# Kernel tuning notes

Measured on AMD Instinct MI355X. Metric: run time of the kernel, lower is better.

The kernel has to match this reference:

```python
import jax, jax.numpy as jnp
import numpy as np

EPS = 1e-5

def _ln(x, g, b):
    mu = x.mean(-1, keepdims=True)
    var = ((x - mu) ** 2).mean(-1, keepdims=True)
    return (x - mu) * jax.lax.rsqrt(var + EPS) * g + b

def setup_inputs() -> dict:
    B, K, D, H, T = 64, 64, 128, 128, 4
    key = jax.random.key(0)
    ks = jax.random.split(key, 20)
    s = 0.02
    inp = {
        "slots": jax.random.normal(ks[0], (B, K, D), jnp.float32),
        "edge_probs": jax.random.uniform(ks[1], (B, K, K), jnp.float32),
        "edge_types": jax.random.uniform(ks[2], (B, K, K, T), jnp.float32),
        # f_self: LayerNorm(D) -> Linear(D,H) -> ReLU -> Linear(H,D)
        "ls_g": jnp.ones((D,), jnp.float32),
        "ls_b": jnp.zeros((D,), jnp.float32),
        "ws1": jax.random.normal(ks[3], (D, H), jnp.float32) * s,
        "bs1": jnp.zeros((H,), jnp.float32),
        "ws2": jax.random.normal(ks[4], (H, D), jnp.float32) * s,
        "bs2": jnp.zeros((D,), jnp.float32),
        # f_inter[tau]: Linear(2D,H) -> ReLU -> Linear(H,H) -> ReLU -> Linear(H,D), stacked over T
        "wi1": jax.random.normal(ks[5], (T, 2 * D, H), jnp.float32) * s,
        "bi1": jnp.zeros((T, H), jnp.float32),
        "wi2": jax.random.normal(ks[6], (T, H, H), jnp.float32) * s,
        "bi2": jnp.zeros((T, H), jnp.float32),
        "wi3": jax.random.normal(ks[7], (T, H, D), jnp.float32) * s,
        "bi3": jnp.zeros((T, D), jnp.float32),
        # update_mlp: LayerNorm(2D) -> Linear(2D,H) -> ReLU -> Linear(H,D)
        "lu_g": jnp.ones((2 * D,), jnp.float32),
        "lu_b": jnp.zeros((2 * D,), jnp.float32),
        "wu1": jax.random.normal(ks[8], (2 * D, H), jnp.float32) * s,
        "bu1": jnp.zeros((H,), jnp.float32),
        "wu2": jax.random.normal(ks[9], (H, D), jnp.float32) * s,
        "bu2": jnp.zeros((D,), jnp.float32),
    }
    return inp

NUM_MP = 2

def reference(slots, edge_probs, edge_types, ls_g, ls_b, ws1, bs1, ws2, bs2,
              wi1, bi1, wi2, bi2, wi3, bi3, lu_g, lu_b, wu1, bu1, wu2, bu2):
    B, K, D = slots.shape
    T = edge_types.shape[-1]
    h = slots
    for _ in range(NUM_MP):
        # f_self
        delta_self = jax.nn.relu(_ln(h, ls_g, ls_b) @ ws1 + bs1) @ ws2 + bs2
        # all-pairs features: cat[b,i,j] = [h[b,i] (sender), h[b,j] (receiver)]
        sender = jnp.broadcast_to(h[:, :, None, :], (B, K, K, D))
        receiver = jnp.broadcast_to(h[:, None, :, :], (B, K, K, D))
        pair = jnp.concatenate([sender, receiver], axis=-1)  # [B,K,K,2D]
        delta_inter = jnp.zeros_like(h)
        for tau in range(T):
            x = jax.nn.relu(pair @ wi1[tau] + bi1[tau])
            x = jax.nn.relu(x @ wi2[tau] + bi2[tau])
            eff = x @ wi3[tau] + bi3[tau]  # [B,K,K,D]
            w = edge_probs[..., None] * edge_types[..., tau, None]  # [B,K,K,1]
            delta_inter = delta_inter + (eff * w).sum(axis=1)  # sum over sender i
        combined = jnp.concatenate([h + delta_self, delta_inter], axis=-1)
        update = jax.nn.relu(_ln(combined, lu_g, lu_b) @ wu1 + bu1) @ wu2 + bu2
        h = h + update  # residual=True
    return h
```

## Files before the change

### kernel.cpp

```cpp
#include <hip/hip_runtime.h>
#include <hip/hip_fp16.h>

#define BATCH 64
#define KSLOT 64
#define DDIM  128
#define HDIM  128
#define TTYPE 4
#define NSLOT (BATCH*KSLOT)
#define EPSLN 1e-5f
#define YROW  544

typedef _Float16 v8h __attribute__((ext_vector_type(8)));
typedef _Float16 v4h __attribute__((ext_vector_type(4)));
typedef float    v4f __attribute__((ext_vector_type(4)));

__device__ __forceinline__ float waveAllSum(float v) {
    #pragma unroll
    for (int m = 1; m < 64; m <<= 1) v += __shfl_xor(v, m, 64);
    return v;
}

__global__ __launch_bounds__(256) void k_wconv(
        const float* __restrict__ ws1, const float* __restrict__ wi1,
        const float* __restrict__ ws2, const float* __restrict__ wu1,
        const float* __restrict__ wu2, const float* __restrict__ wi3,
        const float* __restrict__ wi2, const float* __restrict__ bi1,
        const float* __restrict__ bi3,
        const float* __restrict__ ep, const float* __restrict__ et,
        __half* __restrict__ ws1T, __half* __restrict__ wi1catT,
        __half* __restrict__ ws2T, __half* __restrict__ wu1T,
        __half* __restrict__ wu2T, __half* __restrict__ w3catT,
        __half* __restrict__ w2T16, float* __restrict__ biascat,
        __half* __restrict__ wPre) {
    __shared__ __align__(16) float tile[128*132];
    int bx = blockIdx.x, tid = threadIdx.x;
    if (bx >= 22) {
        int bx2 = bx - 22, tau = bx2 & 3, b = bx2 >> 2;
        const float* epb = ep + (size_t)b*4096;
        const float* etb = et + (size_t)b*4096*TTYPE + tau;
        __half* dst = wPre + ((size_t)tau*BATCH + b)*4096;
        for (int idx = tid; idx < 4096; idx += 256)
            dst[idx] = __float2half(epb[idx] * etb[(size_t)idx*TTYPE]);
        return;
    }
    if (bx == 21) {
        for (int idx = tid; idx < 128*32; idx += 256) {
            int o = idx >> 5, c = idx & 31;
            w3catT[(size_t)o*YROW + 512 + c] = (c < 4) ? __float2half(bi3[c*DDIM + o]) : __float2half(0.f);
        }
        for (int idx = tid; idx < 1024; idx += 256) {
            int th = idx >> 7, o = idx & 127;
            biascat[idx] = (th & 1) ? bi1[(th>>1)*HDIM + o] : 0.f;
        }
        return;
    }
    const float* src; __half* dst; int dstride = 128, dcol = 0;
    if (bx == 0)      { src = ws1; dst = ws1T; }
    else if (bx <= 8) { int th = bx-1, tau = th>>1, half = th&1;
                        src = wi1 + ((size_t)tau*256 + half*128)*128;
                        dst = wi1catT + (size_t)th*128*128; }
    else if (bx == 9) { src = ws2; dst = ws2T; }
    else if (bx ==10) { src = wu2; dst = wu2T; }
    else if (bx <=12) { int hh = bx-11; src = wu1 + (size_t)hh*128*128;
                        dst = wu1T; dstride = 256; dcol = hh*128; }
    else if (bx <=16) { int tau = bx-13; src = wi3 + (size_t)tau*16384;
                        dst = w3catT; dstride = YROW; dcol = tau*128; }
    else              { int tau = bx-17; src = wi2 + (size_t)tau*16384;
                        dst = w2T16 + (size_t)tau*16384; }
    for (int idx = tid; idx < 4096; idx += 256) {
        int r = idx >> 5, c4 = idx & 31;
        *(float4*)&tile[r*132 + c4*4] = *(const float4*)&src[(size_t)r*128 + c4*4];
    }
    __syncthreads();
    for (int idx = tid; idx < 8192; idx += 256) {
        int n = idx >> 6, kp = idx & 63;
        __half2 p = __floats2half2_rn(tile[(2*kp)*132 + n], tile[(2*kp+1)*132 + n]);
        *(__half2*)&dst[(size_t)n*dstride + dcol + 2*kp] = p;
    }
}

__global__ __launch_bounds__(256) void k_front(
        const float* __restrict__ h,
        const __half* __restrict__ wi1catT, const float* __restrict__ biascat,
        const float* __restrict__ ls_g, const float* __restrict__ ls_b,
        const __half* __restrict__ ws1T, const float* __restrict__ bs1,
        const __half* __restrict__ ws2T, const float* __restrict__ bs2,
        __half* __restrict__ AtCt, float* __restrict__ comb128) {
    __shared__ __align__(16) char smem[17152];
    int tid = threadIdx.x, lane = tid & 63, w = tid >> 6;
    int n = lane & 15, quad = lane >> 4;
    int row0 = blockIdx.x*16, nb = blockIdx.y;
    if (nb < 4) {
        _Float16* Ha = (_Float16*)smem;
        for (int u = tid; u < 16*32; u += 256) {
            int r = u >> 5, c4 = (u & 31)*4;
            float4 f = *(const float4*)&h[(size_t)(row0 + r)*128 + c4];
            *(__half2*)&Ha[r*136 + c4]     = __floats2half2_rn(f.x, f.y);
            *(__half2*)&Ha[r*136 + c4 + 2] = __floats2half2_rn(f.z, f.w);
        }
        __syncthreads();
        v8h bfrag[4][4];
        #pragma unroll
        for (int ot = 0; ot < 4; ot++) {
            int col = nb*256 + w*64 + ot*16 + n;
            #pragma unroll
            for (int ks = 0; ks < 4; ks++)
                bfrag[ot][ks] = *(const v8h*)&wi1catT[(size_t)col*128 + ks*32 + quad*8];
        }
        v4f acc[4];
        #pragma unroll
        for (int ot = 0; ot < 4; ot++) {
            float b0 = biascat[nb*256 + w*64 + ot*16 + n];
            acc[ot] = (v4f){b0, b0, b0, b0};
        }
        #pragma unroll
        for (int ks = 0; ks < 4; ks++) {
            v8h a = *(const v8h*)&Ha[n*136 + ks*32 + quad*8];
            #pragma unroll
            for (int ot = 0; ot < 4; ot++)
                acc[ot] = __builtin_amdgcn_mfma_f32_16x16x32_f16(a, bfrag[ot][ks], acc[ot], 0, 0, 0);
        }
        __syncthreads();
        _Float16* Ot = (_Float16*)smem;
        #pragma unroll
        for (int ot = 0; ot < 4; ot++)
            #pragma unroll
            for (int r = 0; r < 4; r++)
                Ot[(quad*4 + r)*264 + w*64 + ot*16 + n] = (_Float16)acc[ot][r];
        __syncthreads();
        #pragma unroll
        for (int u = 0; u < 2; u++) {
            int k = tid + u*256;
            int r = k >> 5, c8 = (k & 31)*8;
            *(v8h*)&AtCt[(size_t)(row0 + r)*1024 + nb*256 + c8] = *(const v8h*)&Ot[r*264 + c8];
        }
    } else {
        float*    Hrow = (float*)smem;
        _Float16* Xa = (_Float16*)(smem + 8448);
        _Float16* Tt = (_Float16*)(smem + 8448 + 4352);
        v8h b1[2][4], b2[2][4];
        #pragma unroll
        for (int ot = 0; ot < 2; ot++) {
            int col = w*32 + ot*16 + n;
            #pragma unroll
            for (int ks = 0; ks < 4; ks++) {
                b1[ot][ks] = *(const v8h*)&ws1T[(size_t)col*128 + ks*32 + quad*8];
                b2[ot][ks] = *(const v8h*)&ws2T[(size_t)col*128 + ks*32 + quad*8];
            }
        }
        for (int u = tid; u < 16*32; u += 256) {
            int r = u >> 5, c4 = (u & 31)*4;
            *(float4*)&Hrow[r*132 + c4] = *(const float4*)&h[(size_t)(row0 + r)*128 + c4];
        }
        __syncthreads();
        #pragma unroll
        for (int rr = 0; rr < 4; rr++) {
            int r = w*4 + rr;
            float x0 = Hrow[r*132 + 2*lane], x1 = Hrow[r*132 + 2*lane + 1];
            float mu = waveAllSum(x0 + x1) * (1.f/128.f);
            float d0 = x0 - mu, d1 = x1 - mu;
            float var = waveAllSum(d0*d0 + d1*d1) * (1.f/128.f);
            float rs = rsqrtf(var + EPSLN);
            float2 gv = *(const float2*)&ls_g[2*lane];
            float2 bv = *(const float2*)&ls_b[2*lane];
            *(__half2*)&Xa[r*136 + 2*lane] = __floats2half2_rn(d0*rs*gv.x + bv.x, d1*rs*gv.y + bv.y);
        }
        __syncthreads();
        v4f acc[2];
        #pragma unroll
        for (int ot = 0; ot < 2; ot++) { float b0 = bs1[w*32 + ot*16 + n]; acc[ot] = (v4f){b0,b0,b0,b0}; }
        #pragma unroll
        for (int ks = 0; ks < 4; ks++) {
            v8h a = *(const v8h*)&Xa[n*136 + ks*32 + quad*8];
            #pragma unroll
            for (int ot = 0; ot < 2; ot++)
                acc[ot] = __builtin_amdgcn_mfma_f32_16x16x32_f16(a, b1[ot][ks], acc[ot], 0, 0, 0);
        }
        #pragma unroll
        for (int ot = 0; ot < 2; ot++)
            #pragma unroll
            for (int r = 0; r < 4; r++)
                Tt[(quad*4 + r)*136 + w*32 + ot*16 + n] = (_Float16)fmaxf(acc[ot][r], 0.f);
        __syncthreads();
        #pragma unroll
        for (int ot = 0; ot < 2; ot++) { float b0 = bs2[w*32 + ot*16 + n]; acc[ot] = (v4f){b0,b0,b0,b0}; }
        #pragma unroll
        for (int ks = 0; ks < 4; ks++) {
            v8h a = *(const v8h*)&Tt[n*136 + ks*32 + quad*8];
            #pragma unroll
            for (int ot = 0; ot < 2; ot++)
                acc[ot] = __builtin_amdgcn_mfma_f32_16x16x32_f16(a, b2[ot][ks], acc[ot], 0, 0, 0);
        }
        #pragma unroll
        for (int ot = 0; ot < 2; ot++)
            #pragma unroll
            for (int r = 0; r < 4; r++) {
                int rr = quad*4 + r, col = w*32 + ot*16 + n;
                comb128[(size_t)(row0 + rr)*128 + col] = Hrow[rr*132 + col] + acc[ot][r];
            }
    }
}

#define LROW 136
__global__ __launch_bounds__(512) void k_pair(
        const __half* __restrict__ AtCt,
        const __half* __restrict__ w2T16,
        const float* __restrict__ bi2,
        const __half* __restrict__ wPre,
        __half* __restrict__ Ycat) {
    __shared__ __align__(16) _Float16 w2T[HDIM*LROW];
    __shared__ __align__(16) _Float16 Cs[KSLOT*LROW];
    __shared__ __align__(16) _Float16 As[KSLOT*LROW];
    __shared__ __align__(16) float    wSf[KSLOT*KSLOT];
    int bx = blockIdx.x, b = bx >> 2, tau = bx & 3;
    int tid = threadIdx.x, lane = tid & 63, w = tid >> 6;
    int jt = w >> 1, oh = w & 1, quad = lane >> 4, n = lane & 15;

    for (int idx = tid; idx < 2048; idx += 512) {
        int o = idx >> 4, seg = (idx & 15)*8;
        *(v8h*)&w2T[o*LROW + seg] = *(const v8h*)&w2T16[((size_t)tau*128 + o)*128 + seg];
    }
    for (int u = tid; u < 1024; u += 512) {
        int j = u >> 4, seg = (u & 15)*8;
        const __half* rp = AtCt + (size_t)(b*KSLOT + j)*1024 + tau*256 + seg;
        *(v8h*)&As[j*LROW + seg] = *(const v8h*)&rp[0];
        *(v8h*)&Cs[j*LROW + seg] = *(const v8h*)&rp[128];
    }
    {
        const __half* wsrc = wPre + ((size_t)tau*BATCH + b)*4096;
        int base = tid*8;
        v8h w8 = *(const v8h*)&wsrc[base];
        #pragma unroll
        for (int q = 0; q < 8; q++) wSf[base + q] = (float)w8[q];
    }
    __syncthreads();

    v8h bfrag[4][4];
    #pragma unroll
    for (int ot = 0; ot < 4; ot++)
        #pragma unroll
        for (int ks = 0; ks < 4; ks++)
            bfrag[ot][ks] = *(const v8h*)&w2T[(oh*64 + ot*16 + n)*LROW + ks*32 + quad*8];
    v8h cfrag[4];
    #pragma unroll
    for (int ks = 0; ks < 4; ks++)
        cfrag[ks] = *(const v8h*)&Cs[(jt*16 + n)*LROW + ks*32 + quad*8];
    float biasv[4];
    #pragma unroll
    for (int ot = 0; ot < 4; ot++) biasv[ot] = bi2[tau*HDIM + oh*64 + ot*16 + n];

    v4f yacc[4];
    #pragma unroll
    for (int ot = 0; ot < 4; ot++) yacc[ot] = (v4f){0.f,0.f,0.f,0.f};
    v4f wsacc = (v4f){0.f,0.f,0.f,0.f};
    const v8h zero8 = {0,0,0,0,0,0,0,0};
    const v4f zero4 = (v4f){0.f,0.f,0.f,0.f};

    v8h aN[4]; v4f wvN;
    #pragma unroll
    for (int ks = 0; ks < 4; ks++) aN[ks] = *(const v8h*)&As[ks*32 + quad*8];
    wvN = *(const v4f*)&wSf[jt*16 + quad*4];

    for (int i = 0; i < KSLOT; ++i) {
        v8h a[4]; v4f wv = wvN;
        #pragma unroll
        for (int ks = 0; ks < 4; ks++) a[ks] = aN[ks];
        if (i < KSLOT-1) {
            #pragma unroll
            for (int ks = 0; ks < 4; ks++)
                aN[ks] = *(const v8h*)&As[(i+1)*LROW + ks*32 + quad*8];
            wvN = *(const v4f*)&wSf[(i+1)*KSLOT + jt*16 + quad*4];
        }
        v8h x1[4];
        #pragma unroll
        for (int ks = 0; ks < 4; ks++)
            x1[ks] = __builtin_elementwise_max(a[ks] + cfrag[ks], zero8);
        #pragma unroll
        for (int ot = 0; ot < 4; ot++) {
            v4f acc = (v4f){biasv[ot], biasv[ot], biasv[ot], biasv[ot]};
            #pragma unroll
            for (int ks = 0; ks < 4; ks++)
                acc = __builtin_amdgcn_mfma_f32_16x16x32_f16(x1[ks], bfrag[ot][ks], acc, 0, 0, 0);
            v4f rel = __builtin_elementwise_max(acc, zero4);
            yacc[ot] = rel*wv + yacc[ot];
        }
        wsacc = wsacc + wv;
    }

    #pragma unroll
    for (int r = 0; r < 4; r++) {
        int j = jt*16 + quad*4 + r;
        __half* yb = Ycat + (size_t)(b*KSLOT + j)*YROW + tau*128 + oh*64;
        #pragma unroll
        for (int ot = 0; ot < 4; ot++)
            yb[ot*16 + n] = __float2half(yacc[ot][r]);
    }
    if (oh == 0 && n == 0) {
        #pragma unroll
        for (int r = 0; r < 4; r++)
            Ycat[(size_t)(b*KSLOT + jt*16 + quad*4 + r)*YROW + 512 + tau] = __float2half(wsacc[r]);
    }
}

__global__ __launch_bounds__(512) void k_mega(
        const __half* __restrict__ Ycat, const __half* __restrict__ w3catT,
        const float* __restrict__ comb128,
        const float* __restrict__ g, const float* __restrict__ bb,
        const __half* __restrict__ wu1T, const float* __restrict__ bu1,
        const __half* __restrict__ wu2T, const float* __restrict__ bu2,
        const float* __restrict__ h, float* __restrict__ hout) {
    __shared__ __align__(16) _Float16 Ys[16*552];
    __shared__ __align__(16) float    Crow[16*260];
    __shared__ __align__(16) _Float16 Xa[16*264];
    __shared__ __align__(16) _Float16 Ut[16*136];
    int tid = threadIdx.x, lane = tid & 63, w = tid >> 6;
    int n = lane & 15, quad = lane >> 4;
    int row0 = blockIdx.x*16;
    for (int u = tid; u < 1024; u += 512) {
        int r = u >> 6, seg = (u & 63)*8;
        *(v8h*)&Ys[r*552 + seg] = *(const v8h*)&Ycat[(size_t)(row0 + r)*YROW + seg];
    }
    if (tid < 64) {
        int r = tid >> 2, seg = 512 + (tid & 3)*8;
        *(v8h*)&Ys[r*552 + seg] = *(const v8h*)&Ycat[(size_t)(row0 + r)*YROW + seg];
    }
    {
        int r = tid >> 5, c4 = (tid & 31)*4;
        *(float4*)&Crow[r*260 + c4] = *(const float4*)&comb128[(size_t)(row0 + r)*128 + c4];
    }
    __syncthreads();
    {
        v4f acc = (v4f){0.f,0.f,0.f,0.f};
        #pragma unroll
        for (int ks = 0; ks < 17; ks++) {
            v8h a = *(const v8h*)&Ys[n*552 + ks*32 + quad*8];
            v8h bfr = *(const v8h*)&w3catT[(size_t)(w*16 + n)*YROW + ks*32 + quad*8];
            acc = __builtin_amdgcn_mfma_f32_16x16x32_f16(a, bfr, acc, 0, 0, 0);
        }
        #pragma unroll
        for (int r = 0; r < 4; r++)
            Crow[(quad*4 + r)*260 + 128 + w*16 + n] = acc[r];
    }
    __syncthreads();
    #pragma unroll
    for (int rr = 0; rr < 2; rr++) {
        int r = w*2 + rr;
        float4 v = *(const float4*)&Crow[r*260 + 4*lane];
        float mu = waveAllSum(v.x + v.y + v.z + v.w) * (1.f/256.f);
        float d0 = v.x-mu, d1 = v.y-mu, d2 = v.z-mu, d3 = v.w-mu;
        float var = waveAllSum(d0*d0 + d1*d1 + d2*d2 + d3*d3) * (1.f/256.f);
        float rs = rsqrtf(var + EPSLN);
        float4 gv = *(const float4*)&g[4*lane];
        float4 bv = *(const float4*)&bb[4*lane];
        *(__half2*)&Xa[r*264 + 4*lane]     = __floats2half2_rn(d0*rs*gv.x + bv.x, d1*rs*gv.y + bv.y);
        *(__half2*)&Xa[r*264 + 4*lane + 2] = __floats2half2_rn(d2*rs*gv.z + bv.z, d3*rs*gv.w + bv.w);
    }
    __syncthreads();
    {
        float b0 = bu1[w*16 + n];
        v4f acc = (v4f){b0, b0, b0, b0};
        #pragma unroll
        for (int ks = 0; ks < 8; ks++) {
            v8h a = *(const v8h*)&Xa[n*264 + ks*32 + quad*8];
            v8h bfr = *(const v8h*)&wu1T[(size_t)(w*16 + n)*256 + ks*32 + quad*8];
            acc = __builtin_amdgcn_mfma_f32_16x16x32_f16(a, bfr, acc, 0, 0, 0);
        }
        #pragma unroll
        for (int r = 0; r < 4; r++)
            Ut[(quad*4 + r)*136 + w*16 + n] = (_Float16)fmaxf(acc[r], 0.f);
    }
    __syncthreads();
    {
        float b0 = bu2[w*16 + n];
        v4f acc = (v4f){b0, b0, b0, b0};
        #pragma unroll
        for (int ks = 0; ks < 4; ks++) {
            v8h a = *(const v8h*)&Ut[n*136 + ks*32 + quad*8];
            v8h bfr = *(const v8h*)&wu2T[(size_t)(w*16 + n)*128 + ks*32 + quad*8];
            acc = __builtin_amdgcn_mfma_f32_16x16x32_f16(a, bfr, acc, 0, 0, 0);
        }
        #pragma unroll
        for (int r = 0; r < 4; r++) {
            int rr = quad*4 + r, col = w*16 + n;
            hout[(size_t)(row0 + rr)*128 + col] = h[(size_t)(row0 + rr)*128 + col] + acc[r];
        }
    }
}

extern "C" void kernel_launch(void* const* d_in, const int* in_sizes, int n_in,
                              void* d_out, int out_size, void* d_ws, size_t ws_size,
                              hipStream_t stream) {
    const float* slots = (const float*)d_in[0];
    const float* ep    = (const float*)d_in[1];
    const float* et    = (const float*)d_in[2];
    const float* ls_g  = (const float*)d_in[3];
    const float* ls_b  = (const float*)d_in[4];
    const float* ws1   = (const float*)d_in[5];
    const float* bs1   = (const float*)d_in[6];
    const float* ws2   = (const float*)d_in[7];
    const float* bs2   = (const float*)d_in[8];
    const float* wi1   = (const float*)d_in[9];
    const float* bi1   = (const float*)d_in[10];
    const float* wi2   = (const float*)d_in[11];
    const float* bi2   = (const float*)d_in[12];
    const float* wi3   = (const float*)d_in[13];
    const float* bi3   = (const float*)d_in[14];
    const float* lu_g  = (const float*)d_in[15];
    const float* lu_b  = (const float*)d_in[16];
    const float* wu1   = (const float*)d_in[17];
    const float* bu1   = (const float*)d_in[18];
    const float* wu2   = (const float*)d_in[19];
    const float* bu2   = (const float*)d_in[20];
    float* out = (float*)d_out;

    char* p = (char*)d_ws;
    float*  h_buf   = (float*)p;   p += (size_t)NSLOT*DDIM*4;
    __half* AtCt    = (__half*)p;  p += (size_t)NSLOT*1024*2;
    __half* Ycat    = (__half*)p;  p += (size_t)NSLOT*YROW*2;
    float*  comb128 = (float*)p;   p += (size_t)NSLOT*128*4;
    __half* wPre    = (__half*)p;  p += (size_t)TTYPE*BATCH*4096*2;
    __half* ws1T    = (__half*)p;  p += 128*128*2;
    __half* wi1catT = (__half*)p;  p += 1024*128*2;
    __half* ws2T    = (__half*)p;  p += 128*128*2;
    __half* wu1T    = (__half*)p;  p += 128*256*2;
    __half* wu2T    = (__half*)p;  p += 128*128*2;
    __half* w3catT  = (__half*)p;  p += 128*YROW*2;
    __half* w2T16   = (__half*)p;  p += 4*128*128*2;
    float*  biascat = (float*)p;   p += 1024*4;

    k_wconv<<<22 + 256, 256, 0, stream>>>(ws1, wi1, ws2, wu1, wu2, wi3, wi2, bi1, bi3,
                                          ep, et, ws1T, wi1catT, ws2T, wu1T, wu2T,
                                          w3catT, w2T16, biascat, wPre);

    for (int mp = 0; mp < 2; mp++) {
        const float* h = (mp == 0) ? slots : h_buf;
        float* hout = (mp == 0) ? h_buf : out;
        k_front<<<dim3(256, 5), 256, 0, stream>>>(h, wi1catT, biascat, ls_g, ls_b,
                                                  ws1T, bs1, ws2T, bs2, AtCt, comb128);
        k_pair<<<BATCH*TTYPE, 512, 0, stream>>>(AtCt, w2T16, bi2, wPre, Ycat);
        k_mega<<<NSLOT/16, 512, 0, stream>>>(Ycat, w3catT, comb128, lu_g, lu_b,
                                             wu1T, bu1, wu2T, bu2, h, hout);
    }
}
```

Before: 232.8 us.

## Accumulate pair-kernel weighted sums in fp16 and prefetch weights before staging loads

The pair kernel now stores edge weights in fp16 shared memory. It converts each MFMA output to packed fp16 with round-toward-zero, applies ReLU, and accumulates the weighted sum in fp16 vectors, which halves the per-iteration epilogue work and shared-memory traffic. Separately, weight fragment loads in the front and mega kernels are moved ahead of activation staging and barriers, and the mega kernel gets a two-blocks launch bound. Accumulating 64 terms in fp16 risks precision loss and overflow, and preloading 29 fragments in the mega kernel raises register pressure.

```diff
diff --git a/kernel.cpp b/kernel.cpp
--- a/kernel.cpp
+++ b/kernel.cpp
@@ -12,6 +12,8 @@
 
 typedef _Float16 v8h __attribute__((ext_vector_type(8)));
 typedef _Float16 v4h __attribute__((ext_vector_type(4)));
+typedef _Float16 v2h __attribute__((ext_vector_type(2)));
+typedef __fp16   v2y __attribute__((ext_vector_type(2)));
 typedef float    v4f __attribute__((ext_vector_type(4)));
 
 __device__ __forceinline__ float waveAllSum(float v) {
@@ -92,6 +94,14 @@
     int row0 = blockIdx.x*16, nb = blockIdx.y;
     if (nb < 4) {
         _Float16* Ha = (_Float16*)smem;
+        v8h bfrag[4][4];
+        #pragma unroll
+        for (int ot = 0; ot < 4; ot++) {
+            int col = nb*256 + w*64 + ot*16 + n;
+            #pragma unroll
+            for (int ks = 0; ks < 4; ks++)
+                bfrag[ot][ks] = *(const v8h*)&wi1catT[(size_t)col*128 + ks*32 + quad*8];
+        }
         for (int u = tid; u < 16*32; u += 256) {
             int r = u >> 5, c4 = (u & 31)*4;
             float4 f = *(const float4*)&h[(size_t)(row0 + r)*128 + c4];
@@ -99,14 +109,6 @@
             *(__half2*)&Ha[r*136 + c4 + 2] = __floats2half2_rn(f.z, f.w);
         }
         __syncthreads();
-        v8h bfrag[4][4];
-        #pragma unroll
-        for (int ot = 0; ot < 4; ot++) {
-            int col = nb*256 + w*64 + ot*16 + n;
-            #pragma unroll
-            for (int ks = 0; ks < 4; ks++)
-                bfrag[ot][ks] = *(const v8h*)&wi1catT[(size_t)col*128 + ks*32 + quad*8];
-        }
         v4f acc[4];
         #pragma unroll
         for (int ot = 0; ot < 4; ot++) {
@@ -211,7 +213,7 @@
     __shared__ __align__(16) _Float16 w2T[HDIM*LROW];
     __shared__ __align__(16) _Float16 Cs[KSLOT*LROW];
     __shared__ __align__(16) _Float16 As[KSLOT*LROW];
-    __shared__ __align__(16) float    wSf[KSLOT*KSLOT];
+    __shared__ __align__(16) _Float16 wS[KSLOT*KSLOT];
     int bx = blockIdx.x, b = bx >> 2, tau = bx & 3;
     int tid = threadIdx.x, lane = tid & 63, w = tid >> 6;
     int jt = w >> 1, oh = w & 1, quad = lane >> 4, n = lane & 15;
@@ -229,9 +231,7 @@
     {
         const __half* wsrc = wPre + ((size_t)tau*BATCH + b)*4096;
         int base = tid*8;
-        v8h w8 = *(const v8h*)&wsrc[base];
-        #pragma unroll
-        for (int q = 0; q < 8; q++) wSf[base + q] = (float)w8[q];
+        *(v8h*)&wS[base] = *(const v8h*)&wsrc[base];
     }
     __syncthreads();
 
@@ -245,31 +245,34 @@
     #pragma unroll
     for (int ks = 0; ks < 4; ks++)
         cfrag[ks] = *(const v8h*)&Cs[(jt*16 + n)*LROW + ks*32 + quad*8];
-    float biasv[4];
-    #pragma unroll
-    for (int ot = 0; ot < 4; ot++) biasv[ot] = bi2[tau*HDIM + oh*64 + ot*16 + n];
-
-    v4f yacc[4];
-    #pragma unroll
-    for (int ot = 0; ot < 4; ot++) yacc[ot] = (v4f){0.f,0.f,0.f,0.f};
-    v4f wsacc = (v4f){0.f,0.f,0.f,0.f};
+    v4f biasvec[4];
+    #pragma unroll
+    for (int ot = 0; ot < 4; ot++) {
+        float b0 = bi2[tau*HDIM + oh*64 + ot*16 + n];
+        biasvec[ot] = (v4f){b0, b0, b0, b0};
+    }
+
+    v4h yacch[4];
+    #pragma unroll
+    for (int ot = 0; ot < 4; ot++) yacch[ot] = (v4h){0,0,0,0};
+    v4h wsacch = (v4h){0,0,0,0};
     const v8h zero8 = {0,0,0,0,0,0,0,0};
-    const v4f zero4 = (v4f){0.f,0.f,0.f,0.f};
-
-    v8h aN[4]; v4f wvN;
+    const v4h zero4h = {0,0,0,0};
+
+    v8h aN[4]; v4h wvN;
     #pragma unroll
     for (int ks = 0; ks < 4; ks++) aN[ks] = *(const v8h*)&As[ks*32 + quad*8];
-    wvN = *(const v4f*)&wSf[jt*16 + quad*4];
+    wvN = *(const v4h*)&wS[jt*16 + quad*4];
 
     for (int i = 0; i < KSLOT; ++i) {
-        v8h a[4]; v4f wv = wvN;
+        v8h a[4]; v4h wv = wvN;
         #pragma unroll
         for (int ks = 0; ks < 4; ks++) a[ks] = aN[ks];
         if (i < KSLOT-1) {
             #pragma unroll
             for (int ks = 0; ks < 4; ks++)
                 aN[ks] = *(const v8h*)&As[(i+1)*LROW + ks*32 + quad*8];
-            wvN = *(const v4f*)&wSf[(i+1)*KSLOT + jt*16 + quad*4];
+            wvN = *(const v4h*)&wS[(i+1)*KSLOT + jt*16 + quad*4];
         }
         v8h x1[4];
         #pragma unroll
@@ -277,14 +280,17 @@
             x1[ks] = __builtin_elementwise_max(a[ks] + cfrag[ks], zero8);
         #pragma unroll
         for (int ot = 0; ot < 4; ot++) {
-            v4f acc = (v4f){biasv[ot], biasv[ot], biasv[ot], biasv[ot]};
-            #pragma unroll
-            for (int ks = 0; ks < 4; ks++)
+            v4f acc = __builtin_amdgcn_mfma_f32_16x16x32_f16(x1[0], bfrag[ot][0], biasvec[ot], 0, 0, 0);
+            #pragma unroll
+            for (int ks = 1; ks < 4; ks++)
                 acc = __builtin_amdgcn_mfma_f32_16x16x32_f16(x1[ks], bfrag[ot][ks], acc, 0, 0, 0);
-            v4f rel = __builtin_elementwise_max(acc, zero4);
-            yacc[ot] = rel*wv + yacc[ot];
-        }
-        wsacc = wsacc + wv;
+            v2h lo = __builtin_bit_cast(v2h, __builtin_amdgcn_cvt_pkrtz(acc[0], acc[1]));
+            v2h hi = __builtin_bit_cast(v2h, __builtin_amdgcn_cvt_pkrtz(acc[2], acc[3]));
+            v4h rel = {lo[0], lo[1], hi[0], hi[1]};
+            rel = __builtin_elementwise_max(rel, zero4h);
+            yacch[ot] = yacch[ot] + wv * rel;
+        }
+        wsacch = wsacch + wv;
     }
 
     #pragma unroll
@@ -293,16 +299,16 @@
         __half* yb = Ycat + (size_t)(b*KSLOT + j)*YROW + tau*128 + oh*64;
         #pragma unroll
         for (int ot = 0; ot < 4; ot++)
-            yb[ot*16 + n] = __float2half(yacc[ot][r]);
+            yb[ot*16 + n] = __float2half((float)yacch[ot][r]);
     }
     if (oh == 0 && n == 0) {
         #pragma unroll
         for (int r = 0; r < 4; r++)
-            Ycat[(size_t)(b*KSLOT + jt*16 + quad*4 + r)*YROW + 512 + tau] = __float2half(wsacc[r]);
-    }
-}
-
-__global__ __launch_bounds__(512) void k_mega(
+            Ycat[(size_t)(b*KSLOT + jt*16 + quad*4 + r)*YROW + 512 + tau] = __float2half((float)wsacch[r]);
+    }
+}
+
+__global__ __launch_bounds__(512, 2) void k_mega(
         const __half* __restrict__ Ycat, const __half* __restrict__ w3catT,
         const float* __restrict__ comb128,
         const float* __restrict__ g, const float* __restrict__ bb,
@@ -316,6 +322,19 @@
     int tid = threadIdx.x, lane = tid & 63, w = tid >> 6;
     int n = lane & 15, quad = lane >> 4;
     int row0 = blockIdx.x*16;
+    v8h f3[17];
+    #pragma unroll
+    for (int ks = 0; ks < 17; ks++)
+        f3[ks] = *(const v8h*)&w3catT[(size_t)(w*16 + n)*YROW + ks*32 + quad*8];
+    v8h f1[8];
+    #pragma unroll
+    for (int ks = 0; ks < 8; ks++)
+        f1[ks] = *(const v8h*)&wu1T[(size_t)(w*16 + n)*256 + ks*32 + quad*8];
+    v8h f2[4];
+    #pragma unroll
+    for (int ks = 0; ks < 4; ks++)
+        f2[ks] = *(const v8h*)&wu2T[(size_t)(w*16 + n)*128 + ks*32 + quad*8];
+
     for (int u = tid; u < 1024; u += 512) {
         int r = u >> 6, seg = (u & 63)*8;
         *(v8h*)&Ys[r*552 + seg] = *(const v8h*)&Ycat[(size_t)(row0 + r)*YROW + seg];
@@ -334,8 +353,7 @@
         #pragma unroll
         for (int ks = 0; ks < 17; ks++) {
             v8h a = *(const v8h*)&Ys[n*552 + ks*32 + quad*8];
-            v8h bfr = *(const v8h*)&w3catT[(size_t)(w*16 + n)*YROW + ks*32 + quad*8];
-            acc = __builtin_amdgcn_mfma_f32_16x16x32_f16(a, bfr, acc, 0, 0, 0);
+            acc = __builtin_amdgcn_mfma_f32_16x16x32_f16(a, f3[ks], acc, 0, 0, 0);
         }
         #pragma unroll
         for (int r = 0; r < 4; r++)
@@ -362,8 +380,7 @@
         #pragma unroll
         for (int ks = 0; ks < 8; ks++) {
             v8h a = *(const v8h*)&Xa[n*264 + ks*32 + quad*8];
-            v8h bfr = *(const v8h*)&wu1T[(size_t)(w*16 + n)*256 + ks*32 + quad*8];
-            acc = __builtin_amdgcn_mfma_f32_16x16x32_f16(a, bfr, acc, 0, 0, 0);
+            acc = __builtin_amdgcn_mfma_f32_16x16x32_f16(a, f1[ks], acc, 0, 0, 0);
         }
         #pragma unroll
         for (int r = 0; r < 4; r++)
@@ -376,8 +393,7 @@
         #pragma unroll
         for (int ks = 0; ks < 4; ks++) {
             v8h a = *(const v8h*)&Ut[n*136 + ks*32 + quad*8];
-            v8h bfr = *(const v8h*)&wu2T[(size_t)(w*16 + n)*128 + ks*32 + quad*8];
-            acc = __builtin_amdgcn_mfma_f32_16x16x32_f16(a, bfr, acc, 0, 0, 0);
+            acc = __builtin_amdgcn_mfma_f32_16x16x32_f16(a, f2[ks], acc, 0, 0, 0);
         }
         #pragma unroll
         for (int r = 0; r < 4; r++) {
```

Result: faster. 219.6 us (-5.7%).
